# Performance work log

Measured on AMD Instinct MI355X. Metric: run time of the kernel, lower is better.

## Reference

```python
import jax, jax.numpy as jnp
import numpy as np

B = 128           # persons in batch
V = 128           # visits per person
CPV = 16          # codes per visit
MAX_VISITS = 510  # 512 - 2, hard-coded in module
D = 256           # embedding_dim * n_heads = 128 * 2
H = 2             # n_heads
DH = D // H
MAX_DAYS = 365
VOCAB = 30000
N_LAYERS = 2
DFF = 4 * D


def setup_inputs() -> dict:
    key = jax.random.key(0)
    ks = jax.random.split(key, 24)
    total_visits = B * V
    total_codes = total_visits * CPV
    all_codes = jax.random.randint(ks[0], (total_codes,), 0, VOCAB, dtype=jnp.int32)
    # code -> visit segment id (contiguous, as produced by the per-person loop)
    seg_ids = (jnp.arange(total_codes, dtype=jnp.int32) // CPV).astype(jnp.int32)
    # visit -> flattened slot in padded [B, MAX_VISITS] tensor (right-aligned)
    pos = MAX_VISITS - V + jnp.arange(V, dtype=jnp.int32)
    dest = (jnp.arange(B, dtype=jnp.int32)[:, None] * MAX_VISITS + pos[None, :]).reshape(-1)
    times = jax.random.uniform(ks[1], (total_visits,), minval=0.0, maxval=float(MAX_DAYS), dtype=jnp.float32)
    s = 0.02
    concept_emb = jax.random.normal(ks[2], (VOCAB, D), dtype=jnp.float32) * s
    pad_emb = jnp.zeros((D,), dtype=jnp.float32)
    Wq = jax.random.normal(ks[3], (N_LAYERS, D, D), dtype=jnp.float32) * s
    Wk = jax.random.normal(ks[4], (N_LAYERS, D, D), dtype=jnp.float32) * s
    Wv = jax.random.normal(ks[5], (N_LAYERS, D, D), dtype=jnp.float32) * s
    Wo = jax.random.normal(ks[6], (N_LAYERS, D, D), dtype=jnp.float32) * s
    W1 = jax.random.normal(ks[7], (N_LAYERS, D, DFF), dtype=jnp.float32) * s
    W2 = jax.random.normal(ks[8], (N_LAYERS, DFF, D), dtype=jnp.float32) * s
    z = lambda *sh: jnp.zeros(sh, dtype=jnp.float32)
    o = lambda *sh: jnp.ones(sh, dtype=jnp.float32)
    return dict(all_codes=all_codes, seg_ids=seg_ids, dest=dest, times=times,
                concept_emb=concept_emb, pad_emb=pad_emb,
                Wq=Wq, Wk=Wk, Wv=Wv, Wo=Wo,
                bq=z(N_LAYERS, D), bk=z(N_LAYERS, D), bv=z(N_LAYERS, D), bo=z(N_LAYERS, D),
                ln1_g=o(N_LAYERS, D), ln1_b=z(N_LAYERS, D),
                W1=W1, b1=z(N_LAYERS, DFF), W2=W2, b2=z(N_LAYERS, D),
                ln2_g=o(N_LAYERS, D), ln2_b=z(N_LAYERS, D))


def _ln(x, g, b):
    m = jnp.mean(x, axis=-1, keepdims=True)
    v = jnp.var(x, axis=-1, keepdims=True)
    return g * (x - m) * jax.lax.rsqrt(v + 1e-5) + b


def _forward(all_codes, seg_ids, dest, times, concept_emb, pad_emb,
             Wq, Wk, Wv, Wo, bq, bk, bv, bo, ln1_g, ln1_b,
             W1, b1, W2, b2, ln2_g, ln2_b):
    # gather code embeddings and segment-sum per visit (index_add_ in torch)
    emb = concept_emb[all_codes]                               # [total_codes, D]
    summed = jax.ops.segment_sum(emb, seg_ids, num_segments=B * V)  # [B*V, D]
    # scatter visits right-aligned into padded [B*MAX_VISITS, D], pad slots = pad_emb
    padded = jnp.broadcast_to(pad_emb, (B * MAX_VISITS, D)).at[dest].set(summed)
    # sinusoidal time embedding: timescales = ((1/1e4)**(1/D))**arange(D/2)
    t = jnp.clip(times, 0.0, float(MAX_DAYS - 1))
    ts = jnp.power(jnp.float32((1.0 / 10000.0) ** (1.0 / D)), jnp.arange(D // 2, dtype=jnp.float32))
    ang = t[:, None] * ts[None, :]                             # [B*V, D/2]
    te = jnp.concatenate([jnp.sin(ang), jnp.cos(ang)], axis=1) # [B*V, D]
    te_pad = jnp.zeros((B * MAX_VISITS, D), dtype=padded.dtype).at[dest].set(te)
    x = (padded + te_pad).reshape(B, MAX_VISITS, D)
    inv_sqrt_dh = np.float32(1.0 / np.sqrt(DH))
    for l in range(N_LAYERS):
        q = (x @ Wq[l] + bq[l]).reshape(B, MAX_VISITS, H, DH)
        k = (x @ Wk[l] + bk[l]).reshape(B, MAX_VISITS, H, DH)
        v = (x @ Wv[l] + bv[l]).reshape(B, MAX_VISITS, H, DH)
        scores = jnp.einsum('bqhd,bkhd->bhqk', q, k) * inv_sqrt_dh
        attn = jax.nn.softmax(scores, axis=-1)
        ctx = jnp.einsum('bhqk,bkhd->bqhd', attn, v).reshape(B, MAX_VISITS, D)
        x = _ln(x + ctx @ Wo[l] + bo[l], ln1_g[l], ln1_b[l])
        ff = jax.nn.relu(x @ W1[l] + b1[l]) @ W2[l] + b2[l]
        x = _ln(x + ff, ln2_g[l], ln2_b[l])
    return x


def reference(all_codes, seg_ids, dest, times, concept_emb, pad_emb,
              Wq, Wk, Wv, Wo, bq, bk, bv, bo, ln1_g, ln1_b,
              W1, b1, W2, b2, ln2_g, ln2_b):
    return _forward(all_codes, seg_ids, dest, times, concept_emb, pad_emb,
                    Wq, Wk, Wv, Wo, bq, bk, bv, bo, ln1_g, ln1_b,
                    W1, b1, W2, b2, ln2_g, ln2_b)
```

## Files before the change

### kernel.cpp

```cpp
#include <hip/hip_runtime.h>
#include <cstddef>

#define BATCH 128
#define NV 128
#define CPV 16
#define MAXV 510
#define SC 256
#define NPAD 382
#define DIM 256
#define NH 2
#define DH 128
#define NLAYERS 2
#define DFF 1024
#define MROWS (BATCH * SC)

typedef __attribute__((ext_vector_type(8))) short short8;
typedef __attribute__((ext_vector_type(4))) short short4v;
typedef __attribute__((ext_vector_type(4))) float floatx4;

__device__ __forceinline__ short f2bf(float f) {
    union { float f; unsigned u; } v; v.f = f;
    unsigned r = v.u + 0x7fffu + ((v.u >> 16) & 1u);
    return (short)(r >> 16);
}
__device__ __forceinline__ float bf2f(short s) {
    union { unsigned u; float f; } v; v.u = ((unsigned)(unsigned short)s) << 16;
    return v.f;
}

__device__ __forceinline__ void gload_lds16(const short* g, short* l) {
    __builtin_amdgcn_global_load_lds(
        (const __attribute__((address_space(1))) unsigned int*)g,
        (__attribute__((address_space(3))) unsigned int*)l,
        16, 0, 0);
}

__global__ __launch_bounds__(256) void wtrans_all(const float* __restrict__ Wq,
                                                  const float* __restrict__ Wk,
                                                  const float* __restrict__ Wv,
                                                  const float* __restrict__ Wo,
                                                  const float* __restrict__ W1,
                                                  const float* __restrict__ W2,
                                                  short* __restrict__ wqkvT,
                                                  short* __restrict__ woT,
                                                  short* __restrict__ w1T,
                                                  short* __restrict__ w2T) {
    int y = blockIdx.y;
    int l = y / 6, w = y - l * 6;
    const float* src; short* dst; int K, nsh;
    switch (w) {
        case 0:  src = Wq + (size_t)l * 65536;  dst = wqkvT + (size_t)l * 196608;           K = 256;  nsh = 8;  break;
        case 1:  src = Wk + (size_t)l * 65536;  dst = wqkvT + (size_t)l * 196608 + 65536;   K = 256;  nsh = 8;  break;
        case 2:  src = Wv + (size_t)l * 65536;  dst = wqkvT + (size_t)l * 196608 + 131072;  K = 256;  nsh = 8;  break;
        case 3:  src = Wo + (size_t)l * 65536;  dst = woT   + (size_t)l * 65536;            K = 256;  nsh = 8;  break;
        case 4:  src = W1 + (size_t)l * 262144; dst = w1T   + (size_t)l * 262144;           K = 256;  nsh = 10; break;
        default: src = W2 + (size_t)l * 262144; dst = w2T   + (size_t)l * 262144;           K = 1024; nsh = 8;  break;
    }
    int N = 1 << nsh;
    int idx = blockIdx.x * 256 + threadIdx.x;
    if (idx >= K * N) return;
    int k = idx >> nsh, n = idx & (N - 1);
    dst[(size_t)n * K + k] = f2bf(src[idx]);
}

__global__ __launch_bounds__(256) void build_x(const int* __restrict__ codes,
                                               const float* __restrict__ times,
                                               const float* __restrict__ cemb,
                                               const float* __restrict__ pemb,
                                               short* __restrict__ x) {
    int row = blockIdx.x;
    int d = threadIdx.x;
    int b = row >> 8;
    int r = row & (SC - 1);
    float val;
    if (r > 128) {
        val = 0.f;
    } else if (r == 128) {
        val = pemb[d];
    } else {
        int visit = b * NV + r;
        const int* cb = codes + visit * CPV;
        float s = 0.f;
#pragma unroll
        for (int c = 0; c < CPV; ++c)
            s += cemb[(size_t)cb[c] * DIM + d];
        float t = times[visit];
        t = fminf(fmaxf(t, 0.f), 364.f);
        int i = d & 127;
        float ang = t * expf(-0.03597789207803197f * (float)i);
        float te = (d < 128) ? sinf(ang) : cosf(ang);
        val = s + te;
    }
    x[(size_t)row * DIM + d] = f2bf(val);
}

__global__ __launch_bounds__(256) void gemm_qkv(const short* __restrict__ A,
                                                const short* __restrict__ BT,
                                                const float* __restrict__ bq,
                                                const float* __restrict__ bk,
                                                const float* __restrict__ bv,
                                                short* __restrict__ qo,
                                                short* __restrict__ ko,
                                                short* __restrict__ vo) {
    __shared__ __align__(16) short lA[128 * 32];
    __shared__ __align__(16) short lB[128 * 32];
    int tid = threadIdx.x;
    int wave = tid >> 6, lane = tid & 63;
    int l15 = lane & 15, quad = lane >> 4;
    int q8 = quad * 8;
    int m0 = blockIdx.y * 128;
    int n0 = blockIdx.x * 128;
    int sel = blockIdx.x >> 1;
    int nloc = n0 & 255;
    int wm = (wave & 1) * 64;
    int wn = (wave >> 1) * 64;

    int srow = tid >> 2;
    int skoff = (tid & 3) * 8;
    const short* ag = A + (size_t)(m0 + srow) * DIM + skoff;
    const short* bg = BT + (size_t)(n0 + srow) * DIM + skoff;
    short* lA_dst = lA + tid * 8;
    short* lB_dst = lB + tid * 8;
    const size_t rstep = (size_t)64 * DIM;

    floatx4 acc[4][4];
#pragma unroll
    for (int i = 0; i < 4; ++i)
#pragma unroll
        for (int j = 0; j < 4; ++j) acc[i][j] = (floatx4){0.f, 0.f, 0.f, 0.f};

#pragma unroll
    for (int k0 = 0; k0 < DIM; k0 += 32) {
        gload_lds16(ag + k0, lA_dst);
        gload_lds16(ag + rstep + k0, lA_dst + 2048);
        gload_lds16(bg + k0, lB_dst);
        gload_lds16(bg + rstep + k0, lB_dst + 2048);
        __syncthreads();
        short8 aF[4], bF[4];
#pragma unroll
        for (int t = 0; t < 4; ++t) {
            aF[t] = *(const short8*)(lA + (wm + t * 16 + l15) * 32 + q8);
            bF[t] = *(const short8*)(lB + (wn + t * 16 + l15) * 32 + q8);
        }
#pragma unroll
        for (int i = 0; i < 4; ++i)
#pragma unroll
            for (int j = 0; j < 4; ++j)
                acc[i][j] = __builtin_amdgcn_mfma_f32_16x16x32_bf16(aF[i], bF[j], acc[i][j], 0, 0, 0);
        __syncthreads();
    }

    const float* bias = (sel == 0) ? bq : (sel == 1) ? bk : bv;
    short* out = (sel == 0) ? qo : (sel == 1) ? ko : vo;
#pragma unroll
    for (int j = 0; j < 4; ++j) {
        int col = nloc + wn + j * 16 + l15;
        float bval = bias[col];
#pragma unroll
        for (int i = 0; i < 4; ++i) {
#pragma unroll
            for (int r = 0; r < 4; ++r) {
                int row = m0 + wm + i * 16 + quad * 4 + r;
                out[(size_t)row * DIM + col] = f2bf(acc[i][j][r] + bval);
            }
        }
    }
}

__global__ __launch_bounds__(256) void gemm_wo_ln(const short* __restrict__ CTX,
                                                  const short* __restrict__ WoT,
                                                  const float* __restrict__ bo,
                                                  const short* __restrict__ X,
                                                  const float* __restrict__ g,
                                                  const float* __restrict__ bta,
                                                  short* __restrict__ xout) {
    __shared__ __align__(16) short lA[64 * 32];
    __shared__ __align__(16) short lB[256 * 32];
    int tid = threadIdx.x;
    int wave = tid >> 6, lane = tid & 63;
    int l15 = lane & 15, quad = lane >> 4;
    int q8 = quad * 8;
    int m0 = blockIdx.x * 64;
    int wr = wave * 16;
    int srow = tid >> 2;
    int skoff = (tid & 3) * 8;
    const short* ag = CTX + (size_t)(m0 + srow) * DIM + skoff;
    const short* bg = WoT + (size_t)srow * DIM + skoff;
    short* lA_dst = lA + tid * 8;
    short* lB_dst = lB + tid * 8;

    floatx4 acc[16];
#pragma unroll
    for (int j = 0; j < 16; ++j) acc[j] = (floatx4){0.f, 0.f, 0.f, 0.f};

#pragma unroll
    for (int k0 = 0; k0 < DIM; k0 += 32) {
        gload_lds16(ag + k0, lA_dst);
        gload_lds16(bg + k0, lB_dst);
        gload_lds16(bg + (size_t)64 * DIM + k0, lB_dst + 2048);
        gload_lds16(bg + (size_t)128 * DIM + k0, lB_dst + 4096);
        gload_lds16(bg + (size_t)192 * DIM + k0, lB_dst + 6144);
        __syncthreads();
        short8 aF = *(const short8*)(lA + (wr + l15) * 32 + q8);
#pragma unroll
        for (int j = 0; j < 16; ++j) {
            short8 bF = *(const short8*)(lB + (j * 16 + l15) * 32 + q8);
            acc[j] = __builtin_amdgcn_mfma_f32_16x16x32_bf16(aF, bF, acc[j], 0, 0, 0);
        }
        __syncthreads();
    }

    float bias[16], gam[16], bet[16];
#pragma unroll
    for (int j = 0; j < 16; ++j) {
        int col = j * 16 + l15;
        bias[j] = bo[col]; gam[j] = g[col]; bet[j] = bta[col];
    }
#pragma unroll
    for (int r = 0; r < 4; ++r) {
        int row = m0 + wr + quad * 4 + r;
        float v[16], s = 0.f, sq = 0.f;
#pragma unroll
        for (int j = 0; j < 16; ++j) {
            v[j] = acc[j][r] + bias[j] + bf2f(X[(size_t)row * DIM + j * 16 + l15]);
            s += v[j]; sq += v[j] * v[j];
        }
        s += __shfl_xor(s, 1); sq += __shfl_xor(sq, 1);
        s += __shfl_xor(s, 2); sq += __shfl_xor(sq, 2);
        s += __shfl_xor(s, 4); sq += __shfl_xor(sq, 4);
        s += __shfl_xor(s, 8); sq += __shfl_xor(sq, 8);
        float mean = s * (1.f / 256.f);
        float var = fmaxf(sq * (1.f / 256.f) - mean * mean, 0.f);
        float rstd = rsqrtf(var + 1e-5f);
#pragma unroll
        for (int j = 0; j < 16; ++j) {
            float y = gam[j] * (v[j] - mean) * rstd + bet[j];
            xout[(size_t)row * DIM + j * 16 + l15] = f2bf(y);
        }
    }
}

#define PST 136
__global__ __launch_bounds__(256, 2) void ff_fused(const short* __restrict__ X,
                                                   const short* __restrict__ W1T,
                                                   const float* __restrict__ b1,
                                                   const short* __restrict__ W2T,
                                                   const float* __restrict__ b2,
                                                   const float* __restrict__ g2,
                                                   const float* __restrict__ bt2,
                                                   short* __restrict__ xout,
                                                   float* __restrict__ fout,
                                                   float* __restrict__ padrow) {
    __shared__ __align__(16) short lA[64 * 32];
    __shared__ __align__(16) short lB[128 * 32];
    __shared__ __align__(16) short lB2[256 * 32];
    __shared__ __align__(16) short lP[64 * PST];
    __shared__ float redS[4][32], redQ[4][32];
    int tid = threadIdx.x;
    int wave = tid >> 6, lane = tid & 63;
    int l15 = lane & 15, quad = lane >> 4;
    int q8 = quad * 8;
    int m0 = blockIdx.x * 64;
    int wm = (wave & 1) * 32;
    int wf = (wave >> 1) * 64;
    int wn2 = (wave >> 1) * 128;
    int srow = tid >> 2;
    int spart = (tid & 3) * 8;
    const short* xg = X + (size_t)(m0 + srow) * DIM + spart;
    short* lA_dst = lA + tid * 8;
    short* lB_dst = lB + tid * 8;
    short* lB2_dst = lB2 + tid * 8;

    floatx4 acc2[2][8];
#pragma unroll
    for (int i = 0; i < 2; ++i)
#pragma unroll
        for (int j = 0; j < 8; ++j) acc2[i][j] = (floatx4){0.f, 0.f, 0.f, 0.f};

    for (int f0 = 0; f0 < DFF; f0 += 128) {
        const short* w1g = W1T + (size_t)(f0 + srow) * DIM + spart;
        floatx4 acc1[2][4];
#pragma unroll
        for (int i = 0; i < 2; ++i)
#pragma unroll
            for (int j = 0; j < 4; ++j) acc1[i][j] = (floatx4){0.f, 0.f, 0.f, 0.f};
#pragma unroll
        for (int k0 = 0; k0 < DIM; k0 += 32) {
            gload_lds16(xg + k0, lA_dst);
            gload_lds16(w1g + k0, lB_dst);
            gload_lds16(w1g + (size_t)64 * DIM + k0, lB_dst + 2048);
            __syncthreads();
            short8 aF[2], bF[4];
#pragma unroll
            for (int t = 0; t < 2; ++t)
                aF[t] = *(const short8*)(lA + (wm + t * 16 + l15) * 32 + q8);
#pragma unroll
            for (int t = 0; t < 4; ++t)
                bF[t] = *(const short8*)(lB + (wf + t * 16 + l15) * 32 + q8);
#pragma unroll
            for (int i = 0; i < 2; ++i)
#pragma unroll
                for (int j = 0; j < 4; ++j)
                    acc1[i][j] = __builtin_amdgcn_mfma_f32_16x16x32_bf16(aF[i], bF[j], acc1[i][j], 0, 0, 0);
            __syncthreads();
        }
#pragma unroll
        for (int j = 0; j < 4; ++j) {
            int fc = wf + j * 16 + l15;
            float bval = b1[f0 + fc];
#pragma unroll
            for (int i = 0; i < 2; ++i) {
#pragma unroll
                for (int r = 0; r < 4; ++r) {
                    float v = acc1[i][j][r] + bval;
                    lP[(wm + i * 16 + quad * 4 + r) * PST + fc] = f2bf(fmaxf(v, 0.f));
                }
            }
        }
        __syncthreads();
#pragma unroll
        for (int ks = 0; ks < 4; ++ks) {
            const short* w2g = W2T + (size_t)srow * DFF + f0 + ks * 32 + spart;
            gload_lds16(w2g, lB2_dst);
            gload_lds16(w2g + (size_t)64 * DFF, lB2_dst + 2048);
            gload_lds16(w2g + (size_t)128 * DFF, lB2_dst + 4096);
            gload_lds16(w2g + (size_t)192 * DFF, lB2_dst + 6144);
            __syncthreads();
            short8 aP[2], bW[8];
#pragma unroll
            for (int t = 0; t < 2; ++t)
                aP[t] = *(const short8*)(lP + (wm + t * 16 + l15) * PST + ks * 32 + q8);
#pragma unroll
            for (int j = 0; j < 8; ++j)
                bW[j] = *(const short8*)(lB2 + (wn2 + j * 16 + l15) * 32 + q8);
#pragma unroll
            for (int i = 0; i < 2; ++i)
#pragma unroll
                for (int j = 0; j < 8; ++j)
                    acc2[i][j] = __builtin_amdgcn_mfma_f32_16x16x32_bf16(aP[i], bW[j], acc2[i][j], 0, 0, 0);
            __syncthreads();
        }
    }

    float b2v[8];
#pragma unroll
    for (int j = 0; j < 8; ++j) b2v[j] = b2[wn2 + j * 16 + l15];
#pragma unroll
    for (int i = 0; i < 2; ++i) {
#pragma unroll
        for (int r = 0; r < 4; ++r) {
            int row = m0 + wm + i * 16 + quad * 4 + r;
            float s = 0.f, sq = 0.f;
#pragma unroll
            for (int j = 0; j < 8; ++j) {
                float v = acc2[i][j][r] + b2v[j] + bf2f(X[(size_t)row * DIM + wn2 + j * 16 + l15]);
                acc2[i][j][r] = v;
                s += v; sq += v * v;
            }
            s += __shfl_xor(s, 1); sq += __shfl_xor(sq, 1);
            s += __shfl_xor(s, 2); sq += __shfl_xor(sq, 2);
            s += __shfl_xor(s, 4); sq += __shfl_xor(sq, 4);
            s += __shfl_xor(s, 8); sq += __shfl_xor(sq, 8);
            if (l15 == 0) {
                int idx = i * 16 + quad * 4 + r;
                redS[wave][idx] = s;
                redQ[wave][idx] = sq;
            }
        }
    }
    __syncthreads();
    float gam[8], bet[8];
#pragma unroll
    for (int j = 0; j < 8; ++j) {
        int col = wn2 + j * 16 + l15;
        gam[j] = g2[col]; bet[j] = bt2[col];
    }
#pragma unroll
    for (int i = 0; i < 2; ++i) {
#pragma unroll
        for (int r = 0; r < 4; ++r) {
            int idx = i * 16 + quad * 4 + r;
            float ts = redS[wave][idx] + redS[wave ^ 2][idx];
            float tq = redQ[wave][idx] + redQ[wave ^ 2][idx];
            float mean = ts * (1.f / 256.f);
            float var = fmaxf(tq * (1.f / 256.f) - mean * mean, 0.f);
            float rstd = rsqrtf(var + 1e-5f);
            int grow = m0 + wm + i * 16 + quad * 4 + r;
            if (!fout) {
#pragma unroll
                for (int j = 0; j < 8; ++j) {
                    float y = gam[j] * (acc2[i][j][r] - mean) * rstd + bet[j];
                    xout[(size_t)grow * DIM + wn2 + j * 16 + l15] = f2bf(y);
                }
            } else {
                int b = grow >> 8, rr = grow & 255;
                if (rr < 128) {
                    float* dst = fout + ((size_t)b * MAXV + NPAD + rr) * DIM;
#pragma unroll
                    for (int j = 0; j < 8; ++j) {
                        float y = gam[j] * (acc2[i][j][r] - mean) * rstd + bet[j];
                        dst[wn2 + j * 16 + l15] = y;
                    }
                } else if (rr == 128) {
#pragma unroll
                    for (int j = 0; j < 8; ++j) {
                        float y = gam[j] * (acc2[i][j][r] - mean) * rstd + bet[j];
                        padrow[(size_t)b * DIM + wn2 + j * 16 + l15] = y;
                    }
                }
            }
        }
    }
}

__global__ __launch_bounds__(256) void pad_bcast(const float* __restrict__ padrow,
                                                 float* __restrict__ fout) {
    int b = blockIdx.y;
    int p = blockIdx.x * 4 + (threadIdx.x >> 6);
    if (p >= NPAD) return;
    int d4 = (threadIdx.x & 63) * 4;
    floatx4 v = *(const floatx4*)(padrow + (size_t)b * DIM + d4);
    *(floatx4*)(fout + ((size_t)b * MAXV + p) * DIM + d4) = v;
}

__global__ __launch_bounds__(256) void transpose_v(const short* __restrict__ v,
                                                   short* __restrict__ vT) {
    __shared__ short lds[32][33];
    int pair = blockIdx.y;
    int b = pair >> 1, h = pair & 1;
    int st = (blockIdx.x & 7) * 32;
    int dt = (blockIdx.x >> 3) * 32;
    int tid = threadIdx.x;
    int sl = tid >> 3, dl = (tid & 7) * 4;
    const short* src = v + ((size_t)(b * SC + st + sl)) * DIM + h * DH + dt + dl;
    short4v val = *(const short4v*)src;
#pragma unroll
    for (int j = 0; j < 4; ++j) lds[sl][dl + j] = val[j];
    __syncthreads();
    int drow = tid >> 3, scol = (tid & 7) * 4;
    short* dst = vT + (size_t)pair * DH * SC + (size_t)(dt + drow) * SC + st + scol;
#pragma unroll
    for (int j = 0; j < 4; ++j) dst[j] = lds[scol + j][drow];
}

#define AST 136
__global__ __launch_bounds__(256) void attn_fused(const short* __restrict__ q,
                                                  const short* __restrict__ k,
                                                  const short* __restrict__ vT,
                                                  short* __restrict__ ctx) {
    __shared__ __align__(16) short lA[128 * 32];
    __shared__ __align__(16) short lB[128 * 32];
    __shared__ __align__(16) short lS[128 * AST];
    int tid = threadIdx.x;
    int wave = tid >> 6, lane = tid & 63;
    int l15 = lane & 15, quad = lane >> 4;
    int q8 = quad * 8;
    int pair = blockIdx.y;
    int b = pair >> 1, h = pair & 1;
    int m0 = blockIdx.x * 128;
    int wm = (wave & 1) * 64;
    int wn = (wave >> 1) * 64;

    const short* Qb = q + ((size_t)b * SC) * DIM + h * DH;
    const short* Kb = k + ((size_t)b * SC) * DIM + h * DH;
    const short* Vb = vT + (size_t)pair * DH * SC;
    int srow = tid >> 2;
    int skoff = (tid & 3) * 8;
    short* lA_dst = lA + tid * 8;
    short* lB_dst = lB + tid * 8;
    const size_t rstep = (size_t)64 * DIM;
    const short* ag = Qb + (size_t)(m0 + srow) * DIM + skoff;
    const float scale = 0.08838834764831845f;

    floatx4 oacc[4][4];
#pragma unroll
    for (int i = 0; i < 4; ++i)
#pragma unroll
        for (int j = 0; j < 4; ++j) oacc[i][j] = (floatx4){0.f, 0.f, 0.f, 0.f};
    float rsum[4] = {0.f, 0.f, 0.f, 0.f};

    for (int kt = 0; kt < 2; ++kt) {
        const short* bg = Kb + (size_t)(kt * 128 + srow) * DIM + skoff;
        floatx4 sacc[4][4];
#pragma unroll
        for (int i = 0; i < 4; ++i)
#pragma unroll
            for (int j = 0; j < 4; ++j) sacc[i][j] = (floatx4){0.f, 0.f, 0.f, 0.f};
#pragma unroll
        for (int k0 = 0; k0 < DH; k0 += 32) {
            gload_lds16(ag + k0, lA_dst);
            gload_lds16(ag + rstep + k0, lA_dst + 2048);
            gload_lds16(bg + k0, lB_dst);
            gload_lds16(bg + rstep + k0, lB_dst + 2048);
            __syncthreads();
            short8 aF[4], bF[4];
#pragma unroll
            for (int t = 0; t < 4; ++t) {
                aF[t] = *(const short8*)(lA + (wm + t * 16 + l15) * 32 + q8);
                bF[t] = *(const short8*)(lB + (wn + t * 16 + l15) * 32 + q8);
            }
#pragma unroll
            for (int i = 0; i < 4; ++i)
#pragma unroll
                for (int j = 0; j < 4; ++j)
                    sacc[i][j] = __builtin_amdgcn_mfma_f32_16x16x32_bf16(aF[i], bF[j], sacc[i][j], 0, 0, 0);
            __syncthreads();
        }
#pragma unroll
        for (int j = 0; j < 4; ++j) {
            int col = wn + j * 16 + l15;
            int cg = kt * 128 + col;
            float w = (cg < 128) ? 1.f : ((cg == 128) ? (float)NPAD : 0.f);
#pragma unroll
            for (int i = 0; i < 4; ++i) {
#pragma unroll
                for (int r = 0; r < 4; ++r) {
                    float e = __expf(fminf(sacc[i][j][r] * scale, 30.f));
                    lS[(wm + i * 16 + quad * 4 + r) * AST + col] = f2bf(w * e);
                }
            }
        }
        __syncthreads();
#pragma unroll
        for (int ks = 0; ks < 4; ++ks) {
            const short* vg = Vb + (size_t)srow * SC + kt * 128 + ks * 32 + skoff;
            gload_lds16(vg, lB_dst);
            gload_lds16(vg + (size_t)64 * SC, lB_dst + 2048);
            __syncthreads();
            short8 aP[4], bV[4];
#pragma unroll
            for (int t = 0; t < 4; ++t) {
                aP[t] = *(const short8*)(lS + (wm + t * 16 + l15) * AST + ks * 32 + q8);
                bV[t] = *(const short8*)(lB + (wn + t * 16 + l15) * 32 + q8);
            }
#pragma unroll
            for (int i = 0; i < 4; ++i) {
                float s = 0.f;
#pragma unroll
                for (int e = 0; e < 8; ++e) s += bf2f(aP[i][e]);
                rsum[i] += s;
            }
#pragma unroll
            for (int i = 0; i < 4; ++i)
#pragma unroll
                for (int j = 0; j < 4; ++j)
                    oacc[i][j] = __builtin_amdgcn_mfma_f32_16x16x32_bf16(aP[i], bV[j], oacc[i][j], 0, 0, 0);
            __syncthreads();
        }
    }

#pragma unroll
    for (int i = 0; i < 4; ++i) {
        rsum[i] += __shfl_xor(rsum[i], 16);
        rsum[i] += __shfl_xor(rsum[i], 32);
    }
    short* outb = ctx + ((size_t)(b * SC + m0)) * DIM + h * DH;
#pragma unroll
    for (int i = 0; i < 4; ++i) {
#pragma unroll
        for (int r = 0; r < 4; ++r) {
            float inv = 1.f / __shfl(rsum[i], quad * 4 + r);
#pragma unroll
            for (int j = 0; j < 4; ++j) {
                int col = wn + j * 16 + l15;
                int row = wm + i * 16 + quad * 4 + r;
                outb[(size_t)row * DIM + col] = f2bf(oacc[i][j][r] * inv);
            }
        }
    }
}

extern "C" void kernel_launch(void* const* d_in, const int* in_sizes, int n_in,
                              void* d_out, int out_size, void* d_ws, size_t ws_size,
                              hipStream_t stream) {
    const int*   all_codes = (const int*)d_in[0];
    const float* times = (const float*)d_in[3];
    const float* cemb  = (const float*)d_in[4];
    const float* pemb  = (const float*)d_in[5];
    const float* Wq = (const float*)d_in[6];
    const float* Wk = (const float*)d_in[7];
    const float* Wv = (const float*)d_in[8];
    const float* Wo = (const float*)d_in[9];
    const float* bq = (const float*)d_in[10];
    const float* bk = (const float*)d_in[11];
    const float* bv = (const float*)d_in[12];
    const float* bo = (const float*)d_in[13];
    const float* ln1g = (const float*)d_in[14];
    const float* ln1b = (const float*)d_in[15];
    const float* W1 = (const float*)d_in[16];
    const float* b1 = (const float*)d_in[17];
    const float* W2 = (const float*)d_in[18];
    const float* b2 = (const float*)d_in[19];
    const float* ln2g = (const float*)d_in[20];
    const float* ln2b = (const float*)d_in[21];

    char* ws = (char*)d_ws;
    short* wqkvT = (short*)ws;
    short* woT   = wqkvT + 2 * 196608;
    short* w1T   = woT + 2 * 65536;
    short* w2T   = w1T + 2 * 262144;
    float* padrow = (float*)(ws + (3500u << 10));

    const size_t SLOT = (size_t)MROWS * DIM;
    short* xb = (short*)(ws + (4u << 20));
    short* C0 = xb + SLOT;
    short* C1 = C0 + SLOT;
    short* C2 = C1 + SLOT;
    short* C3 = C2 + SLOT;
    short* C4 = C3 + SLOT;

    wtrans_all<<<dim3(1024, 12), 256, 0, stream>>>(Wq, Wk, Wv, Wo, W1, W2,
                                                   wqkvT, woT, w1T, w2T);
    build_x<<<MROWS, 256, 0, stream>>>(all_codes, times, cemb, pemb, xb);

    for (int l = 0; l < NLAYERS; ++l) {
        const short* qkv_l = wqkvT + (size_t)l * 196608;
        const short* wo_l = woT + (size_t)l * 65536;
        const short* w1_l = w1T + (size_t)l * 262144;
        const short* w2_l = w2T + (size_t)l * 262144;
        int last = (l == NLAYERS - 1);

        gemm_qkv<<<dim3(6, MROWS / 128), 256, 0, stream>>>(xb, qkv_l, bq + l * 256, bk + l * 256,
                                                           bv + l * 256, C0, C1, C2);
        transpose_v<<<dim3(32, BATCH * NH), 256, 0, stream>>>(C2, C4);
        attn_fused<<<dim3(2, BATCH * NH), 256, 0, stream>>>(C0, C1, C4, C3);
        gemm_wo_ln<<<MROWS / 64, 256, 0, stream>>>(C3, wo_l, bo + l * 256, xb,
                                                   ln1g + l * 256, ln1b + l * 256, C0);
        ff_fused<<<MROWS / 64, 256, 0, stream>>>(C0, w1_l, b1 + l * 1024, w2_l, b2 + l * 256,
                                                 ln2g + l * 256, ln2b + l * 256, xb,
                                                 last ? (float*)d_out : nullptr,
                                                 last ? padrow : nullptr);
        if (last)
            pad_bcast<<<dim3(96, BATCH), 256, 0, stream>>>(padrow, (float*)d_out);
    }
}
```

Baseline: 468.1 us.

## Double-buffer LDS tiles in QKV, Wo+LN and fused FFN GEMMs

Converts the three GEMM kernels from single-buffered LDS staging to ping-pong double buffering. The next K-slice is loaded into the alternate buffer while MFMAs run on the current one, and one of the two barriers per iteration is removed. The fused FFN also prefetches the first W2 slice while the ReLU tile is written. This doubles LDS use, which may cut occupancy, notably for ff_fused with its launch bound of 2 blocks per CU. It also depends on the direct global-to-LDS loads completing correctly behind a single barrier.

```diff
diff --git a/kernel.cpp b/kernel.cpp
--- a/kernel.cpp
+++ b/kernel.cpp
@@ -102,8 +102,8 @@
                                                 short* __restrict__ qo,
                                                 short* __restrict__ ko,
                                                 short* __restrict__ vo) {
-    __shared__ __align__(16) short lA[128 * 32];
-    __shared__ __align__(16) short lB[128 * 32];
+    __shared__ __align__(16) short lA[2][128 * 32];
+    __shared__ __align__(16) short lB[2][128 * 32];
     int tid = threadIdx.x;
     int wave = tid >> 6, lane = tid & 63;
     int l15 = lane & 15, quad = lane >> 4;
@@ -119,9 +119,8 @@
     int skoff = (tid & 3) * 8;
     const short* ag = A + (size_t)(m0 + srow) * DIM + skoff;
     const short* bg = BT + (size_t)(n0 + srow) * DIM + skoff;
-    short* lA_dst = lA + tid * 8;
-    short* lB_dst = lB + tid * 8;
     const size_t rstep = (size_t)64 * DIM;
+    int t8 = tid * 8;
 
     floatx4 acc[4][4];
 #pragma unroll
@@ -129,18 +128,26 @@
 #pragma unroll
         for (int j = 0; j < 4; ++j) acc[i][j] = (floatx4){0.f, 0.f, 0.f, 0.f};
 
-#pragma unroll
-    for (int k0 = 0; k0 < DIM; k0 += 32) {
-        gload_lds16(ag + k0, lA_dst);
-        gload_lds16(ag + rstep + k0, lA_dst + 2048);
-        gload_lds16(bg + k0, lB_dst);
-        gload_lds16(bg + rstep + k0, lB_dst + 2048);
-        __syncthreads();
+    gload_lds16(ag, lA[0] + t8);
+    gload_lds16(ag + rstep, lA[0] + 2048 + t8);
+    gload_lds16(bg, lB[0] + t8);
+    gload_lds16(bg + rstep, lB[0] + 2048 + t8);
+    __syncthreads();
+    int cur = 0;
+#pragma unroll
+    for (int k0 = 0; k0 < 8; ++k0) {
+        if (k0 < 7) {
+            int kn = (k0 + 1) * 32;
+            gload_lds16(ag + kn, lA[cur ^ 1] + t8);
+            gload_lds16(ag + rstep + kn, lA[cur ^ 1] + 2048 + t8);
+            gload_lds16(bg + kn, lB[cur ^ 1] + t8);
+            gload_lds16(bg + rstep + kn, lB[cur ^ 1] + 2048 + t8);
+        }
         short8 aF[4], bF[4];
 #pragma unroll
         for (int t = 0; t < 4; ++t) {
-            aF[t] = *(const short8*)(lA + (wm + t * 16 + l15) * 32 + q8);
-            bF[t] = *(const short8*)(lB + (wn + t * 16 + l15) * 32 + q8);
+            aF[t] = *(const short8*)(lA[cur] + (wm + t * 16 + l15) * 32 + q8);
+            bF[t] = *(const short8*)(lB[cur] + (wn + t * 16 + l15) * 32 + q8);
         }
 #pragma unroll
         for (int i = 0; i < 4; ++i)
@@ -148,6 +155,7 @@
             for (int j = 0; j < 4; ++j)
                 acc[i][j] = __builtin_amdgcn_mfma_f32_16x16x32_bf16(aF[i], bF[j], acc[i][j], 0, 0, 0);
         __syncthreads();
+        cur ^= 1;
     }
 
     const float* bias = (sel == 0) ? bq : (sel == 1) ? bk : bv;
@@ -174,8 +182,8 @@
                                                   const float* __restrict__ g,
                                                   const float* __restrict__ bta,
                                                   short* __restrict__ xout) {
-    __shared__ __align__(16) short lA[64 * 32];
-    __shared__ __align__(16) short lB[256 * 32];
+    __shared__ __align__(16) short lA[2][64 * 32];
+    __shared__ __align__(16) short lB[2][256 * 32];
     int tid = threadIdx.x;
     int wave = tid >> 6, lane = tid & 63;
     int l15 = lane & 15, quad = lane >> 4;
@@ -186,28 +194,37 @@
     int skoff = (tid & 3) * 8;
     const short* ag = CTX + (size_t)(m0 + srow) * DIM + skoff;
     const short* bg = WoT + (size_t)srow * DIM + skoff;
-    short* lA_dst = lA + tid * 8;
-    short* lB_dst = lB + tid * 8;
+    int t8 = tid * 8;
 
     floatx4 acc[16];
 #pragma unroll
     for (int j = 0; j < 16; ++j) acc[j] = (floatx4){0.f, 0.f, 0.f, 0.f};
 
-#pragma unroll
-    for (int k0 = 0; k0 < DIM; k0 += 32) {
-        gload_lds16(ag + k0, lA_dst);
-        gload_lds16(bg + k0, lB_dst);
-        gload_lds16(bg + (size_t)64 * DIM + k0, lB_dst + 2048);
-        gload_lds16(bg + (size_t)128 * DIM + k0, lB_dst + 4096);
-        gload_lds16(bg + (size_t)192 * DIM + k0, lB_dst + 6144);
+    gload_lds16(ag, lA[0] + t8);
+    gload_lds16(bg, lB[0] + t8);
+    gload_lds16(bg + (size_t)64 * DIM, lB[0] + 2048 + t8);
+    gload_lds16(bg + (size_t)128 * DIM, lB[0] + 4096 + t8);
+    gload_lds16(bg + (size_t)192 * DIM, lB[0] + 6144 + t8);
+    __syncthreads();
+    int cur = 0;
+#pragma unroll
+    for (int k0 = 0; k0 < 8; ++k0) {
+        if (k0 < 7) {
+            int kn = (k0 + 1) * 32;
+            gload_lds16(ag + kn, lA[cur ^ 1] + t8);
+            gload_lds16(bg + kn, lB[cur ^ 1] + t8);
+            gload_lds16(bg + (size_t)64 * DIM + kn, lB[cur ^ 1] + 2048 + t8);
+            gload_lds16(bg + (size_t)128 * DIM + kn, lB[cur ^ 1] + 4096 + t8);
+            gload_lds16(bg + (size_t)192 * DIM + kn, lB[cur ^ 1] + 6144 + t8);
+        }
+        short8 aF = *(const short8*)(lA[cur] + (wr + l15) * 32 + q8);
+#pragma unroll
+        for (int j = 0; j < 16; ++j) {
+            short8 bF = *(const short8*)(lB[cur] + (j * 16 + l15) * 32 + q8);
+            acc[j] = __builtin_amdgcn_mfma_f32_16x16x32_bf16(aF, bF, acc[j], 0, 0, 0);
+        }
         __syncthreads();
-        short8 aF = *(const short8*)(lA + (wr + l15) * 32 + q8);
-#pragma unroll
-        for (int j = 0; j < 16; ++j) {
-            short8 bF = *(const short8*)(lB + (j * 16 + l15) * 32 + q8);
-            acc[j] = __builtin_amdgcn_mfma_f32_16x16x32_bf16(aF, bF, acc[j], 0, 0, 0);
-        }
-        __syncthreads();
+        cur ^= 1;
     }
 
     float bias[16], gam[16], bet[16];
@@ -251,9 +268,9 @@
                                                    short* __restrict__ xout,
                                                    float* __restrict__ fout,
                                                    float* __restrict__ padrow) {
-    __shared__ __align__(16) short lA[64 * 32];
-    __shared__ __align__(16) short lB[128 * 32];
-    __shared__ __align__(16) short lB2[256 * 32];
+    __shared__ __align__(16) short lA[2][64 * 32];
+    __shared__ __align__(16) short lB[2][128 * 32];
+    __shared__ __align__(16) short lB2[2][256 * 32];
     __shared__ __align__(16) short lP[64 * PST];
     __shared__ float redS[4][32], redQ[4][32];
     int tid = threadIdx.x;
@@ -267,9 +284,7 @@
     int srow = tid >> 2;
     int spart = (tid & 3) * 8;
     const short* xg = X + (size_t)(m0 + srow) * DIM + spart;
-    short* lA_dst = lA + tid * 8;
-    short* lB_dst = lB + tid * 8;
-    short* lB2_dst = lB2 + tid * 8;
+    int t8 = tid * 8;
 
     floatx4 acc2[2][8];
 #pragma unroll
@@ -284,25 +299,42 @@
         for (int i = 0; i < 2; ++i)
 #pragma unroll
             for (int j = 0; j < 4; ++j) acc1[i][j] = (floatx4){0.f, 0.f, 0.f, 0.f};
-#pragma unroll
-        for (int k0 = 0; k0 < DIM; k0 += 32) {
-            gload_lds16(xg + k0, lA_dst);
-            gload_lds16(w1g + k0, lB_dst);
-            gload_lds16(w1g + (size_t)64 * DIM + k0, lB_dst + 2048);
-            __syncthreads();
+
+        gload_lds16(xg, lA[0] + t8);
+        gload_lds16(w1g, lB[0] + t8);
+        gload_lds16(w1g + (size_t)64 * DIM, lB[0] + 2048 + t8);
+        __syncthreads();
+        int cur = 0;
+#pragma unroll
+        for (int k0 = 0; k0 < 8; ++k0) {
+            if (k0 < 7) {
+                int kn = (k0 + 1) * 32;
+                gload_lds16(xg + kn, lA[cur ^ 1] + t8);
+                gload_lds16(w1g + kn, lB[cur ^ 1] + t8);
+                gload_lds16(w1g + (size_t)64 * DIM + kn, lB[cur ^ 1] + 2048 + t8);
+            }
             short8 aF[2], bF[4];
 #pragma unroll
             for (int t = 0; t < 2; ++t)
-                aF[t] = *(const short8*)(lA + (wm + t * 16 + l15) * 32 + q8);
+                aF[t] = *(const short8*)(lA[cur] + (wm + t * 16 + l15) * 32 + q8);
 #pragma unroll
             for (int t = 0; t < 4; ++t)
-                bF[t] = *(const short8*)(lB + (wf + t * 16 + l15) * 32 + q8);
+                bF[t] = *(const short8*)(lB[cur] + (wf + t * 16 + l15) * 32 + q8);
 #pragma unroll
             for (int i = 0; i < 2; ++i)
 #pragma unroll
                 for (int j = 0; j < 4; ++j)
                     acc1[i][j] = __builtin_amdgcn_mfma_f32_16x16x32_bf16(aF[i], bF[j], acc1[i][j], 0, 0, 0);
             __syncthreads();
+            cur ^= 1;
+        }
+
+        {
+            const short* w2g = W2T + (size_t)srow * DFF + f0 + spart;
+            gload_lds16(w2g, lB2[0] + t8);
+            gload_lds16(w2g + (size_t)64 * DFF, lB2[0] + 2048 + t8);
+            gload_lds16(w2g + (size_t)128 * DFF, lB2[0] + 4096 + t8);
+            gload_lds16(w2g + (size_t)192 * DFF, lB2[0] + 6144 + t8);
         }
 #pragma unroll
         for (int j = 0; j < 4; ++j) {
@@ -318,27 +350,30 @@
             }
         }
         __syncthreads();
+        cur = 0;
 #pragma unroll
         for (int ks = 0; ks < 4; ++ks) {
-            const short* w2g = W2T + (size_t)srow * DFF + f0 + ks * 32 + spart;
-            gload_lds16(w2g, lB2_dst);
-            gload_lds16(w2g + (size_t)64 * DFF, lB2_dst + 2048);
-            gload_lds16(w2g + (size_t)128 * DFF, lB2_dst + 4096);
-            gload_lds16(w2g + (size_t)192 * DFF, lB2_dst + 6144);
-            __syncthreads();
+            if (ks < 3) {
+                const short* w2g = W2T + (size_t)srow * DFF + f0 + (ks + 1) * 32 + spart;
+                gload_lds16(w2g, lB2[cur ^ 1] + t8);
+                gload_lds16(w2g + (size_t)64 * DFF, lB2[cur ^ 1] + 2048 + t8);
+                gload_lds16(w2g + (size_t)128 * DFF, lB2[cur ^ 1] + 4096 + t8);
+                gload_lds16(w2g + (size_t)192 * DFF, lB2[cur ^ 1] + 6144 + t8);
+            }
             short8 aP[2], bW[8];
 #pragma unroll
             for (int t = 0; t < 2; ++t)
                 aP[t] = *(const short8*)(lP + (wm + t * 16 + l15) * PST + ks * 32 + q8);
 #pragma unroll
             for (int j = 0; j < 8; ++j)
-                bW[j] = *(const short8*)(lB2 + (wn2 + j * 16 + l15) * 32 + q8);
+                bW[j] = *(const short8*)(lB2[cur] + (wn2 + j * 16 + l15) * 32 + q8);
 #pragma unroll
             for (int i = 0; i < 2; ++i)
 #pragma unroll
                 for (int j = 0; j < 8; ++j)
                     acc2[i][j] = __builtin_amdgcn_mfma_f32_16x16x32_bf16(aP[i], bW[j], acc2[i][j], 0, 0, 0);
             __syncthreads();
+            cur ^= 1;
         }
     }
 
```

After: 458.7 us. -2.0%, faster.

## Load MFMA operands directly from global memory instead of LDS staging

Applied to the files above, without the earlier changes.

Every GEMM and attention kernel now loads its MFMA fragments straight from global memory into registers. The earlier global_load_lds staging into shared memory is gone, along with most of the per-k-step barriers. This is meant to remove LDS traffic and synchronisation stalls and to free shared memory for higher occupancy. The cost is that operands shared across waves are fetched redundantly through the caches, and each lane issues narrow 16-byte loads that are less coalesced across rows.

```diff
diff --git a/kernel.cpp b/kernel.cpp
--- a/kernel.cpp
+++ b/kernel.cpp
@@ -26,13 +26,6 @@
 __device__ __forceinline__ float bf2f(short s) {
     union { unsigned u; float f; } v; v.u = ((unsigned)(unsigned short)s) << 16;
     return v.f;
-}
-
-__device__ __forceinline__ void gload_lds16(const short* g, short* l) {
-    __builtin_amdgcn_global_load_lds(
-        (const __attribute__((address_space(1))) unsigned int*)g,
-        (__attribute__((address_space(3))) unsigned int*)l,
-        16, 0, 0);
 }
 
 __global__ __launch_bounds__(256) void wtrans_all(const float* __restrict__ Wq,
@@ -102,8 +95,6 @@
                                                 short* __restrict__ qo,
                                                 short* __restrict__ ko,
                                                 short* __restrict__ vo) {
-    __shared__ __align__(16) short lA[128 * 32];
-    __shared__ __align__(16) short lB[128 * 32];
     int tid = threadIdx.x;
     int wave = tid >> 6, lane = tid & 63;
     int l15 = lane & 15, quad = lane >> 4;
@@ -115,13 +106,8 @@
     int wm = (wave & 1) * 64;
     int wn = (wave >> 1) * 64;
 
-    int srow = tid >> 2;
-    int skoff = (tid & 3) * 8;
-    const short* ag = A + (size_t)(m0 + srow) * DIM + skoff;
-    const short* bg = BT + (size_t)(n0 + srow) * DIM + skoff;
-    short* lA_dst = lA + tid * 8;
-    short* lB_dst = lB + tid * 8;
-    const size_t rstep = (size_t)64 * DIM;
+    const short* a0 = A  + (size_t)(m0 + wm + l15) * DIM + q8;
+    const short* b0 = BT + (size_t)(n0 + wn + l15) * DIM + q8;
 
     floatx4 acc[4][4];
 #pragma unroll
@@ -131,23 +117,17 @@
 
 #pragma unroll
     for (int k0 = 0; k0 < DIM; k0 += 32) {
-        gload_lds16(ag + k0, lA_dst);
-        gload_lds16(ag + rstep + k0, lA_dst + 2048);
-        gload_lds16(bg + k0, lB_dst);
-        gload_lds16(bg + rstep + k0, lB_dst + 2048);
-        __syncthreads();
         short8 aF[4], bF[4];
 #pragma unroll
         for (int t = 0; t < 4; ++t) {
-            aF[t] = *(const short8*)(lA + (wm + t * 16 + l15) * 32 + q8);
-            bF[t] = *(const short8*)(lB + (wn + t * 16 + l15) * 32 + q8);
+            aF[t] = *(const short8*)(a0 + (size_t)t * 16 * DIM + k0);
+            bF[t] = *(const short8*)(b0 + (size_t)t * 16 * DIM + k0);
         }
 #pragma unroll
         for (int i = 0; i < 4; ++i)
 #pragma unroll
             for (int j = 0; j < 4; ++j)
                 acc[i][j] = __builtin_amdgcn_mfma_f32_16x16x32_bf16(aF[i], bF[j], acc[i][j], 0, 0, 0);
-        __syncthreads();
     }
 
     const float* bias = (sel == 0) ? bq : (sel == 1) ? bk : bv;
@@ -174,20 +154,15 @@
                                                   const float* __restrict__ g,
                                                   const float* __restrict__ bta,
                                                   short* __restrict__ xout) {
-    __shared__ __align__(16) short lA[64 * 32];
-    __shared__ __align__(16) short lB[256 * 32];
     int tid = threadIdx.x;
     int wave = tid >> 6, lane = tid & 63;
     int l15 = lane & 15, quad = lane >> 4;
     int q8 = quad * 8;
     int m0 = blockIdx.x * 64;
     int wr = wave * 16;
-    int srow = tid >> 2;
-    int skoff = (tid & 3) * 8;
-    const short* ag = CTX + (size_t)(m0 + srow) * DIM + skoff;
-    const short* bg = WoT + (size_t)srow * DIM + skoff;
-    short* lA_dst = lA + tid * 8;
-    short* lB_dst = lB + tid * 8;
+
+    const short* a0 = CTX + (size_t)(m0 + wr + l15) * DIM + q8;
+    const short* b0 = WoT + (size_t)l15 * DIM + q8;
 
     floatx4 acc[16];
 #pragma unroll
@@ -195,19 +170,12 @@
 
 #pragma unroll
     for (int k0 = 0; k0 < DIM; k0 += 32) {
-        gload_lds16(ag + k0, lA_dst);
-        gload_lds16(bg + k0, lB_dst);
-        gload_lds16(bg + (size_t)64 * DIM + k0, lB_dst + 2048);
-        gload_lds16(bg + (size_t)128 * DIM + k0, lB_dst + 4096);
-        gload_lds16(bg + (size_t)192 * DIM + k0, lB_dst + 6144);
-        __syncthreads();
-        short8 aF = *(const short8*)(lA + (wr + l15) * 32 + q8);
+        short8 aF = *(const short8*)(a0 + k0);
 #pragma unroll
         for (int j = 0; j < 16; ++j) {
-            short8 bF = *(const short8*)(lB + (j * 16 + l15) * 32 + q8);
+            short8 bF = *(const short8*)(b0 + (size_t)j * 16 * DIM + k0);
             acc[j] = __builtin_amdgcn_mfma_f32_16x16x32_bf16(aF, bF, acc[j], 0, 0, 0);
         }
-        __syncthreads();
     }
 
     float bias[16], gam[16], bet[16];
@@ -241,19 +209,16 @@
 }
 
 #define PST 136
-__global__ __launch_bounds__(256, 2) void ff_fused(const short* __restrict__ X,
-                                                   const short* __restrict__ W1T,
-                                                   const float* __restrict__ b1,
-                                                   const short* __restrict__ W2T,
-                                                   const float* __restrict__ b2,
-                                                   const float* __restrict__ g2,
-                                                   const float* __restrict__ bt2,
-                                                   short* __restrict__ xout,
-                                                   float* __restrict__ fout,
-                                                   float* __restrict__ padrow) {
-    __shared__ __align__(16) short lA[64 * 32];
-    __shared__ __align__(16) short lB[128 * 32];
-    __shared__ __align__(16) short lB2[256 * 32];
+__global__ __launch_bounds__(256) void ff_fused(const short* __restrict__ X,
+                                                const short* __restrict__ W1T,
+                                                const float* __restrict__ b1,
+                                                const short* __restrict__ W2T,
+                                                const float* __restrict__ b2,
+                                                const float* __restrict__ g2,
+                                                const float* __restrict__ bt2,
+                                                short* __restrict__ xout,
+                                                float* __restrict__ fout,
+                                                float* __restrict__ padrow) {
     __shared__ __align__(16) short lP[64 * PST];
     __shared__ float redS[4][32], redQ[4][32];
     int tid = threadIdx.x;
@@ -264,12 +229,9 @@
     int wm = (wave & 1) * 32;
     int wf = (wave >> 1) * 64;
     int wn2 = (wave >> 1) * 128;
-    int srow = tid >> 2;
-    int spart = (tid & 3) * 8;
-    const short* xg = X + (size_t)(m0 + srow) * DIM + spart;
-    short* lA_dst = lA + tid * 8;
-    short* lB_dst = lB + tid * 8;
-    short* lB2_dst = lB2 + tid * 8;
+
+    const short* x0 = X + (size_t)(m0 + wm + l15) * DIM + q8;
+    const short* w2 = W2T + (size_t)(wn2 + l15) * DFF + q8;
 
     floatx4 acc2[2][8];
 #pragma unroll
@@ -278,32 +240,30 @@
         for (int j = 0; j < 8; ++j) acc2[i][j] = (floatx4){0.f, 0.f, 0.f, 0.f};
 
     for (int f0 = 0; f0 < DFF; f0 += 128) {
-        const short* w1g = W1T + (size_t)(f0 + srow) * DIM + spart;
+        const short* w1 = W1T + (size_t)(f0 + wf + l15) * DIM + q8;
         floatx4 acc1[2][4];
 #pragma unroll
         for (int i = 0; i < 2; ++i)
 #pragma unroll
             for (int j = 0; j < 4; ++j) acc1[i][j] = (floatx4){0.f, 0.f, 0.f, 0.f};
+
 #pragma unroll
         for (int k0 = 0; k0 < DIM; k0 += 32) {
-            gload_lds16(xg + k0, lA_dst);
-            gload_lds16(w1g + k0, lB_dst);
-            gload_lds16(w1g + (size_t)64 * DIM + k0, lB_dst + 2048);
-            __syncthreads();
             short8 aF[2], bF[4];
 #pragma unroll
             for (int t = 0; t < 2; ++t)
-                aF[t] = *(const short8*)(lA + (wm + t * 16 + l15) * 32 + q8);
+                aF[t] = *(const short8*)(x0 + (size_t)t * 16 * DIM + k0);
 #pragma unroll
             for (int t = 0; t < 4; ++t)
-                bF[t] = *(const short8*)(lB + (wf + t * 16 + l15) * 32 + q8);
+                bF[t] = *(const short8*)(w1 + (size_t)t * 16 * DIM + k0);
 #pragma unroll
             for (int i = 0; i < 2; ++i)
 #pragma unroll
                 for (int j = 0; j < 4; ++j)
                     acc1[i][j] = __builtin_amdgcn_mfma_f32_16x16x32_bf16(aF[i], bF[j], acc1[i][j], 0, 0, 0);
-            __syncthreads();
-        }
+        }
+
+        __syncthreads();
 #pragma unroll
         for (int j = 0; j < 4; ++j) {
             int fc = wf + j * 16 + l15;
@@ -318,30 +278,25 @@
             }
         }
         __syncthreads();
+
 #pragma unroll
         for (int ks = 0; ks < 4; ++ks) {
-            const short* w2g = W2T + (size_t)srow * DFF + f0 + ks * 32 + spart;
-            gload_lds16(w2g, lB2_dst);
-            gload_lds16(w2g + (size_t)64 * DFF, lB2_dst + 2048);
-            gload_lds16(w2g + (size_t)128 * DFF, lB2_dst + 4096);
-            gload_lds16(w2g + (size_t)192 * DFF, lB2_dst + 6144);
-            __syncthreads();
             short8 aP[2], bW[8];
 #pragma unroll
             for (int t = 0; t < 2; ++t)
                 aP[t] = *(const short8*)(lP + (wm + t * 16 + l15) * PST + ks * 32 + q8);
 #pragma unroll
             for (int j = 0; j < 8; ++j)
-                bW[j] = *(const short8*)(lB2 + (wn2 + j * 16 + l15) * 32 + q8);
+                bW[j] = *(const short8*)(w2 + (size_t)j * 16 * DFF + f0 + ks * 32);
 #pragma unroll
             for (int i = 0; i < 2; ++i)
 #pragma unroll
                 for (int j = 0; j < 8; ++j)
                     acc2[i][j] = __builtin_amdgcn_mfma_f32_16x16x32_bf16(aP[i], bW[j], acc2[i][j], 0, 0, 0);
-            __syncthreads();
-        }
-    }
-
+        }
+    }
+
+    __syncthreads();
     float b2v[8];
 #pragma unroll
     for (int j = 0; j < 8; ++j) b2v[j] = b2[wn2 + j * 16 + l15];
@@ -448,8 +403,6 @@
                                                   const short* __restrict__ k,
                                                   const short* __restrict__ vT,
                                                   short* __restrict__ ctx) {
-    __shared__ __align__(16) short lA[128 * 32];
-    __shared__ __align__(16) short lB[128 * 32];
     __shared__ __align__(16) short lS[128 * AST];
     int tid = threadIdx.x;
     int wave = tid >> 6, lane = tid & 63;
@@ -461,15 +414,9 @@
     int wm = (wave & 1) * 64;
     int wn = (wave >> 1) * 64;
 
-    const short* Qb = q + ((size_t)b * SC) * DIM + h * DH;
-    const short* Kb = k + ((size_t)b * SC) * DIM + h * DH;
-    const short* Vb = vT + (size_t)pair * DH * SC;
-    int srow = tid >> 2;
-    int skoff = (tid & 3) * 8;
-    short* lA_dst = lA + tid * 8;
-    short* lB_dst = lB + tid * 8;
-    const size_t rstep = (size_t)64 * DIM;
-    const short* ag = Qb + (size_t)(m0 + srow) * DIM + skoff;
+    const short* q0 = q  + ((size_t)(b * SC + m0 + wm + l15)) * DIM + h * DH + q8;
+    const short* k0p = k + ((size_t)(b * SC + wn + l15)) * DIM + h * DH + q8;
+    const short* v0 = vT + (size_t)pair * DH * SC + (size_t)(wn + l15) * SC + q8;
     const float scale = 0.08838834764831845f;
 
     floatx4 oacc[4][4];
@@ -480,32 +427,26 @@
     float rsum[4] = {0.f, 0.f, 0.f, 0.f};
 
     for (int kt = 0; kt < 2; ++kt) {
-        const short* bg = Kb + (size_t)(kt * 128 + srow) * DIM + skoff;
         floatx4 sacc[4][4];
 #pragma unroll
         for (int i = 0; i < 4; ++i)
 #pragma unroll
             for (int j = 0; j < 4; ++j) sacc[i][j] = (floatx4){0.f, 0.f, 0.f, 0.f};
 #pragma unroll
-        for (int k0 = 0; k0 < DH; k0 += 32) {
-            gload_lds16(ag + k0, lA_dst);
-            gload_lds16(ag + rstep + k0, lA_dst + 2048);
-            gload_lds16(bg + k0, lB_dst);
-            gload_lds16(bg + rstep + k0, lB_dst + 2048);
-            __syncthreads();
+        for (int c0 = 0; c0 < DH; c0 += 32) {
             short8 aF[4], bF[4];
 #pragma unroll
             for (int t = 0; t < 4; ++t) {
-                aF[t] = *(const short8*)(lA + (wm + t * 16 + l15) * 32 + q8);
-                bF[t] = *(const short8*)(lB + (wn + t * 16 + l15) * 32 + q8);
+                aF[t] = *(const short8*)(q0 + (size_t)t * 16 * DIM + c0);
+                bF[t] = *(const short8*)(k0p + (size_t)(kt * 128 + t * 16) * DIM + c0);
             }
 #pragma unroll
             for (int i = 0; i < 4; ++i)
 #pragma unroll
                 for (int j = 0; j < 4; ++j)
                     sacc[i][j] = __builtin_amdgcn_mfma_f32_16x16x32_bf16(aF[i], bF[j], sacc[i][j], 0, 0, 0);
-            __syncthreads();
-        }
+        }
+        __syncthreads();
 #pragma unroll
         for (int j = 0; j < 4; ++j) {
             int col = wn + j * 16 + l15;
@@ -523,15 +464,11 @@
         __syncthreads();
 #pragma unroll
         for (int ks = 0; ks < 4; ++ks) {
-            const short* vg = Vb + (size_t)srow * SC + kt * 128 + ks * 32 + skoff;
-            gload_lds16(vg, lB_dst);
-            gload_lds16(vg + (size_t)64 * SC, lB_dst + 2048);
-            __syncthreads();
             short8 aP[4], bV[4];
 #pragma unroll
             for (int t = 0; t < 4; ++t) {
                 aP[t] = *(const short8*)(lS + (wm + t * 16 + l15) * AST + ks * 32 + q8);
-                bV[t] = *(const short8*)(lB + (wn + t * 16 + l15) * 32 + q8);
+                bV[t] = *(const short8*)(v0 + (size_t)t * 16 * SC + kt * 128 + ks * 32);
             }
 #pragma unroll
             for (int i = 0; i < 4; ++i) {
@@ -545,7 +482,6 @@
 #pragma unroll
                 for (int j = 0; j < 4; ++j)
                     oacc[i][j] = __builtin_amdgcn_mfma_f32_16x16x32_bf16(aP[i], bV[j], oacc[i][j], 0, 0, 0);
-            __syncthreads();
         }
     }
 
```

Result: slower. 721.3 us (+54.1%).
